# Optimization experiments

Measured on AMD Instinct MI355X. Metric: run time of the kernel, lower is better.

The kernel has to match this reference:

```python
import jax, jax.numpy as jnp
import numpy as np

N = 100000
E = 1600000
IN_C = 128
OUT_C = 64


def setup_inputs() -> dict:
    key = jax.random.key(0)
    ks = jax.random.split(key, 8)
    x = jax.random.normal(ks[0], (N, IN_C), dtype=jnp.float32)
    edge_index = jax.random.randint(ks[1], (2, E), 0, N, dtype=jnp.int64)
    neg_edge_index = jax.random.randint(ks[2], (2, E), 0, N, dtype=jnp.int64)
    # GCNConv params (glorot-ish init)
    W = jax.random.normal(ks[3], (IN_C, OUT_C), dtype=jnp.float32) / np.sqrt(IN_C)
    b = jnp.zeros((OUT_C,), dtype=jnp.float32)
    # classifier Linear(2*out_channels, 2)
    Wc = jax.random.normal(ks[4], (2 * OUT_C, 2), dtype=jnp.float32) / np.sqrt(2 * OUT_C)
    bc = jnp.zeros((2,), dtype=jnp.float32)
    return {"x": x, "edge_index": edge_index, "neg_edge_index": neg_edge_index,
            "W": W, "b": b, "Wc": Wc, "bc": bc}


def gcn_conv(x, edge_index, W, b):
    # Add self-loops, symmetric normalization: D^{-1/2} (A+I) D^{-1/2} X W + b
    loops = jnp.arange(N, dtype=edge_index.dtype)
    src = jnp.concatenate([edge_index[0], loops])  # [E+N]
    dst = jnp.concatenate([edge_index[1], loops])  # [E+N]
    deg = jax.ops.segment_sum(jnp.ones_like(dst, dtype=x.dtype), dst, num_segments=N)
    dinv = jax.lax.rsqrt(jnp.maximum(deg, 1e-12))
    norm = dinv[src] * dinv[dst]                   # [E+N]
    xw = x @ W                                     # [N, OUT_C] transform first (cheaper)
    msg = norm[:, None] * xw[src]                  # gather + scale
    out = jax.ops.segment_sum(msg, dst, num_segments=N)  # scatter-add aggregate
    return out + b


def reference(x, edge_index, neg_edge_index, W, b, Wc, bc):
    h = jax.nn.relu(gcn_conv(x, edge_index, W, b))           # [N, OUT_C]
    total = jnp.concatenate([edge_index, neg_edge_index], axis=1)  # [2, 2E]
    edge_feat = jnp.concatenate([h[total[0]], h[total[1]]], axis=1)  # [2E, 2*OUT_C]
    return edge_feat @ Wc + bc                               # [2E, 2]
```

## Files before the change

### kernel.cpp

```cpp
#include <hip/hip_runtime.h>

#define N_NODES 100000
#define N_EDGES 1600000
#define IN_C    128
#define OUT_C   64

#define SB_NODES 512
#define NSB  ((N_NODES + SB_NODES - 1) / SB_NODES)
#define SCAP 9216
#define ACHUNK 2048
#define NABLK ((N_EDGES + ACHUNK - 1) / ACHUNK)

__device__ inline unsigned pack_bf16x2(float lo, float hi) {
    unsigned a = __float_as_uint(lo), b2 = __float_as_uint(hi);
    a  += 0x7fff + ((a  >> 16) & 1);
    b2 += 0x7fff + ((b2 >> 16) & 1);
    return (a >> 16) | (b2 & 0xffff0000u);
}
__device__ inline float bf_lo(unsigned v) { return __uint_as_float(v << 16); }
__device__ inline float bf_hi(unsigned v) { return __uint_as_float(v & 0xffff0000u); }

__global__ void zero_kernel(int* __restrict__ cursor) {
    int i = blockIdx.x * blockDim.x + threadIdx.x;
    if (i < NSB) cursor[i] = 0;
}

__global__ __launch_bounds__(256) void sorta_kernel(const int* __restrict__ ei,
                                                    int* __restrict__ cursor,
                                                    int* __restrict__ sb) {
    __shared__ int histW[4][NSB];
    __shared__ int base_[NSB];
    __shared__ int cur[NSB];
    const int t = threadIdx.x, w = t >> 6;
    const long long e0 = (long long)blockIdx.x * ACHUNK;
    for (int i = t; i < 4 * NSB; i += 256) (&histW[0][0])[i] = 0;
    __syncthreads();
    const int* dsts = ei + N_EDGES;
#pragma unroll
    for (int k = 0; k < ACHUNK / 1024; ++k) {
        long long i4 = e0 / 4 + t + k * 256;
        if (i4 * 4 + 3 < N_EDGES) {
            int4 d = *(const int4*)&dsts[i4 * 4];
            atomicAdd(&histW[w][d.x >> 9], 1);
            atomicAdd(&histW[w][d.y >> 9], 1);
            atomicAdd(&histW[w][d.z >> 9], 1);
            atomicAdd(&histW[w][d.w >> 9], 1);
        }
    }
    __syncthreads();
    if (t < NSB) {
        int c = histW[0][t] + histW[1][t] + histW[2][t] + histW[3][t];
        base_[t] = c ? atomicAdd(&cursor[t], c) : 0;
        cur[t] = 0;
    }
    __syncthreads();
#pragma unroll
    for (int k = 0; k < ACHUNK / 1024; ++k) {
        long long i4 = e0 / 4 + t + k * 256;
        if (i4 * 4 + 3 < N_EDGES) {
            int4 s4 = *(const int4*)&ei[i4 * 4];
            int4 d4 = *(const int4*)&dsts[i4 * 4];
            int sv[4] = {s4.x, s4.y, s4.z, s4.w};
            int dv[4] = {d4.x, d4.y, d4.z, d4.w};
#pragma unroll
            for (int j = 0; j < 4; ++j) {
                int bk = dv[j] >> 9;
                int pos = base_[bk] + atomicAdd(&cur[bk], 1);
                if (pos < SCAP)
                    sb[bk * SCAP + pos] = sv[j] * SB_NODES + (dv[j] & (SB_NODES - 1));
            }
        }
    }
}

__global__ __launch_bounds__(1024) void sortb_kernel(const int* __restrict__ cursor,
                                                     int* __restrict__ sb,
                                                     float* __restrict__ dinv,
                                                     int* __restrict__ rowbeg,
                                                     int* __restrict__ rowend) {
    __shared__ int hist[SB_NODES];
    __shared__ int pref[SB_NODES + 1];
    __shared__ int cur[SB_NODES];
    __shared__ int sc[SB_NODES];
    __shared__ int sorted[SCAP];
    const int t = threadIdx.x, b = blockIdx.x;
    if (t < SB_NODES) { hist[t] = 0; cur[t] = 0; }
    __syncthreads();
    int m = cursor[b]; if (m > SCAP) m = SCAP;
    int* bb = sb + b * SCAP;
    for (int i = t; i < m; i += 1024) atomicAdd(&hist[bb[i] & (SB_NODES - 1)], 1);
    __syncthreads();
    if (t < SB_NODES) sc[t] = hist[t];
    __syncthreads();
    for (int off = 1; off < SB_NODES; off <<= 1) {
        int u = 0;
        if (t < SB_NODES && t >= off) u = sc[t - off];
        __syncthreads();
        if (t < SB_NODES) sc[t] += u;
        __syncthreads();
    }
    if (t < SB_NODES) pref[t] = sc[t] - hist[t];
    if (t == SB_NODES - 1) pref[SB_NODES] = sc[SB_NODES - 1];
    __syncthreads();
    for (int i = t; i < m; i += 1024) {
        int e = bb[i];
        int dl = e & (SB_NODES - 1);
        int pos = pref[dl] + atomicAdd(&cur[dl], 1);
        sorted[pos] = e >> 9;
    }
    __syncthreads();
    for (int i = t; i < m; i += 1024) bb[i] = sorted[i];
    if (t < SB_NODES) {
        int n = b * SB_NODES + t;
        if (n < N_NODES) {
            rowbeg[n] = b * SCAP + pref[t];
            rowend[n] = b * SCAP + pref[t + 1];
            dinv[n]   = rsqrtf((float)hist[t] + 1.0f);
        }
    }
}

#define XN  32
#define SXS 132
__global__ __launch_bounds__(256) void xws_kernel(const float* __restrict__ x,
                                                  const float* __restrict__ W,
                                                  const float* __restrict__ dinv,
                                                  unsigned* __restrict__ xwsh) {
    __shared__ float sW[IN_C * OUT_C];
    __shared__ float sx[XN * SXS];
    const int t = threadIdx.x;
    const int n0 = blockIdx.x * XN;
    const float4* W4 = (const float4*)W;
    float4* sW4 = (float4*)sW;
#pragma unroll
    for (int k = 0; k < 8; ++k) sW4[t + k * 256] = W4[t + k * 256];
#pragma unroll
    for (int k = 0; k < 4; ++k) {
        int idx = (t + k * 256) * 4;
        int r = idx >> 7, kk = idx & 127;
        int n = n0 + r;
        float4 v = (n < N_NODES) ? *(const float4*)&x[(long long)n * IN_C + kk]
                                 : make_float4(0.f, 0.f, 0.f, 0.f);
        *(float4*)&sx[r * SXS + kk] = v;
    }
    __syncthreads();
    const int r  = t >> 4;
    const int cq = (t & 15) << 2;
    float4 a0 = make_float4(0.f,0.f,0.f,0.f), a1 = a0;
#pragma unroll 8
    for (int k = 0; k < IN_C; ++k) {
        float x0 = sx[r * SXS + k];
        float x1 = sx[(r + 16) * SXS + k];
        float4 wv = *(const float4*)&sW[(k << 6) + cq];
        a0.x = fmaf(x0, wv.x, a0.x); a0.y = fmaf(x0, wv.y, a0.y);
        a0.z = fmaf(x0, wv.z, a0.z); a0.w = fmaf(x0, wv.w, a0.w);
        a1.x = fmaf(x1, wv.x, a1.x); a1.y = fmaf(x1, wv.y, a1.y);
        a1.z = fmaf(x1, wv.z, a1.z); a1.w = fmaf(x1, wv.w, a1.w);
    }
    int na = n0 + r, nb = n0 + r + 16;
    if (na < N_NODES) {
        float di = dinv[na];
        uint2 o = make_uint2(pack_bf16x2(a0.x * di, a0.y * di),
                             pack_bf16x2(a0.z * di, a0.w * di));
        *(uint2*)&xwsh[(long long)na * 32 + ((t & 15) << 1)] = o;
    }
    if (nb < N_NODES) {
        float di = dinv[nb];
        uint2 o = make_uint2(pack_bf16x2(a1.x * di, a1.y * di),
                             pack_bf16x2(a1.z * di, a1.w * di));
        *(uint2*)&xwsh[(long long)nb * 32 + ((t & 15) << 1)] = o;
    }
}

__global__ __launch_bounds__(256) void aggnode_kernel(
    const int* __restrict__ rowbeg, const int* __restrict__ rowend,
    const int* __restrict__ srcs, const float* __restrict__ dinv,
    const unsigned* __restrict__ xwsh, const float* __restrict__ b,
    const float* __restrict__ Wc, const float* __restrict__ bc,
    float2* __restrict__ p, float2* __restrict__ q) {
    const int lane = threadIdx.x & 63;
    const int hl   = lane & 31;
    const int g    = hl >> 3;
    const int j    = hl & 7;
    const unsigned woff = (unsigned)(j << 2);
    const int node = blockIdx.x * 8 + ((threadIdx.x >> 6) << 1) + (lane >> 5);
    const int beg = rowbeg[node], end = rowend[node];
    const float di = dinv[node];
    const uint4 vsl = *(const uint4*)&xwsh[((unsigned)node << 5) + woff];
    float a0=0.f,a1=0.f,a2=0.f,a3=0.f,a4=0.f,a5=0.f,a6=0.f,a7=0.f;
    const int m1 = end - 1;
    for (int i = beg; i < end; i += 16) {
        int e0 = i + g, e1 = e0 + 4, e2 = e0 + 8, e3 = e0 + 12;
        int i0 = min(e0, m1), i1 = min(e1, m1), i2 = min(e2, m1), i3 = min(e3, m1);
        int s0 = srcs[i0], s1 = srcs[i1], s2 = srcs[i2], s3 = srcs[i3];
        float f0 = (e0 < end) ? 1.f : 0.f;
        float f1 = (e1 < end) ? 1.f : 0.f;
        float f2 = (e2 < end) ? 1.f : 0.f;
        float f3 = (e3 < end) ? 1.f : 0.f;
        uint4 v0 = *(const uint4*)&xwsh[((unsigned)s0 << 5) + woff];
        uint4 v1 = *(const uint4*)&xwsh[((unsigned)s1 << 5) + woff];
        uint4 v2 = *(const uint4*)&xwsh[((unsigned)s2 << 5) + woff];
        uint4 v3 = *(const uint4*)&xwsh[((unsigned)s3 << 5) + woff];
        a0 = fmaf(f0, bf_lo(v0.x), a0); a1 = fmaf(f0, bf_hi(v0.x), a1);
        a2 = fmaf(f0, bf_lo(v0.y), a2); a3 = fmaf(f0, bf_hi(v0.y), a3);
        a4 = fmaf(f0, bf_lo(v0.z), a4); a5 = fmaf(f0, bf_hi(v0.z), a5);
        a6 = fmaf(f0, bf_lo(v0.w), a6); a7 = fmaf(f0, bf_hi(v0.w), a7);
        a0 = fmaf(f1, bf_lo(v1.x), a0); a1 = fmaf(f1, bf_hi(v1.x), a1);
        a2 = fmaf(f1, bf_lo(v1.y), a2); a3 = fmaf(f1, bf_hi(v1.y), a3);
        a4 = fmaf(f1, bf_lo(v1.z), a4); a5 = fmaf(f1, bf_hi(v1.z), a5);
        a6 = fmaf(f1, bf_lo(v1.w), a6); a7 = fmaf(f1, bf_hi(v1.w), a7);
        a0 = fmaf(f2, bf_lo(v2.x), a0); a1 = fmaf(f2, bf_hi(v2.x), a1);
        a2 = fmaf(f2, bf_lo(v2.y), a2); a3 = fmaf(f2, bf_hi(v2.y), a3);
        a4 = fmaf(f2, bf_lo(v2.z), a4); a5 = fmaf(f2, bf_hi(v2.z), a5);
        a6 = fmaf(f2, bf_lo(v2.w), a6); a7 = fmaf(f2, bf_hi(v2.w), a7);
        a0 = fmaf(f3, bf_lo(v3.x), a0); a1 = fmaf(f3, bf_hi(v3.x), a1);
        a2 = fmaf(f3, bf_lo(v3.y), a2); a3 = fmaf(f3, bf_hi(v3.y), a3);
        a4 = fmaf(f3, bf_lo(v3.z), a4); a5 = fmaf(f3, bf_hi(v3.z), a5);
        a6 = fmaf(f3, bf_lo(v3.w), a6); a7 = fmaf(f3, bf_hi(v3.w), a7);
    }
    a0 += __shfl_xor(a0, 8); a0 += __shfl_xor(a0, 16);
    a1 += __shfl_xor(a1, 8); a1 += __shfl_xor(a1, 16);
    a2 += __shfl_xor(a2, 8); a2 += __shfl_xor(a2, 16);
    a3 += __shfl_xor(a3, 8); a3 += __shfl_xor(a3, 16);
    a4 += __shfl_xor(a4, 8); a4 += __shfl_xor(a4, 16);
    a5 += __shfl_xor(a5, 8); a5 += __shfl_xor(a5, 16);
    a6 += __shfl_xor(a6, 8); a6 += __shfl_xor(a6, 16);
    a7 += __shfl_xor(a7, 8); a7 += __shfl_xor(a7, 16);
    a0 += bf_lo(vsl.x); a1 += bf_hi(vsl.x);
    a2 += bf_lo(vsl.y); a3 += bf_hi(vsl.y);
    a4 += bf_lo(vsl.z); a5 += bf_hi(vsl.z);
    a6 += bf_lo(vsl.w); a7 += bf_hi(vsl.w);
    float4 bA = ((const float4*)b)[(j << 1)];
    float4 bB = ((const float4*)b)[(j << 1) + 1];
    float h0 = fmaxf(fmaf(di, a0, bA.x), 0.f);
    float h1 = fmaxf(fmaf(di, a1, bA.y), 0.f);
    float h2 = fmaxf(fmaf(di, a2, bA.z), 0.f);
    float h3 = fmaxf(fmaf(di, a3, bA.w), 0.f);
    float h4 = fmaxf(fmaf(di, a4, bB.x), 0.f);
    float h5 = fmaxf(fmaf(di, a5, bB.y), 0.f);
    float h6 = fmaxf(fmaf(di, a6, bB.z), 0.f);
    float h7 = fmaxf(fmaf(di, a7, bB.w), 0.f);
    const float4* WS = (const float4*)Wc;
    const float4* WD = (const float4*)(Wc + 2 * OUT_C);
    float p0, p1, q0, q1;
    {
        float4 w0 = WS[(j << 2)], w1 = WS[(j << 2) + 1];
        float4 w2 = WS[(j << 2) + 2], w3 = WS[(j << 2) + 3];
        p0 = h0 * w0.x + h1 * w0.z + h2 * w1.x + h3 * w1.z
           + h4 * w2.x + h5 * w2.z + h6 * w3.x + h7 * w3.z;
        p1 = h0 * w0.y + h1 * w0.w + h2 * w1.y + h3 * w1.w
           + h4 * w2.y + h5 * w2.w + h6 * w3.y + h7 * w3.w;
    }
    {
        float4 u0 = WD[(j << 2)], u1 = WD[(j << 2) + 1];
        float4 u2 = WD[(j << 2) + 2], u3 = WD[(j << 2) + 3];
        q0 = h0 * u0.x + h1 * u0.z + h2 * u1.x + h3 * u1.z
           + h4 * u2.x + h5 * u2.z + h6 * u3.x + h7 * u3.z;
        q1 = h0 * u0.y + h1 * u0.w + h2 * u1.y + h3 * u1.w
           + h4 * u2.y + h5 * u2.w + h6 * u3.y + h7 * u3.w;
    }
#pragma unroll
    for (int off = 1; off <= 4; off <<= 1) {
        p0 += __shfl_xor(p0, off); p1 += __shfl_xor(p1, off);
        q0 += __shfl_xor(q0, off); q1 += __shfl_xor(q1, off);
    }
    if (hl == 0) {
        p[node] = make_float2(p0 + bc[0], p1 + bc[1]);
        q[node] = make_float2(q0, q1);
    }
}

__global__ __launch_bounds__(256) void edge_kernel(
    const int* __restrict__ ei, const int* __restrict__ nei,
    const float2* __restrict__ p, const float2* __restrict__ q,
    float4* __restrict__ out4) {
    int idx = blockIdx.x * blockDim.x + threadIdx.x;
    if (idx >= 2 * N_EDGES / 8) return;
    int e8 = idx * 8;
    const int *S, *D;
    int off;
    if (e8 < N_EDGES) { S = ei;  D = ei  + N_EDGES; off = e8; }
    else              { S = nei; D = nei + N_EDGES; off = e8 - N_EDGES; }
    int4 sA = *(const int4*)&S[off];
    int4 sB = *(const int4*)&S[off + 4];
    int4 dA = *(const int4*)&D[off];
    int4 dB = *(const int4*)&D[off + 4];
    float2 p0 = p[sA.x], p1 = p[sA.y], p2 = p[sA.z], p3 = p[sA.w];
    float2 p4 = p[sB.x], p5 = p[sB.y], p6 = p[sB.z], p7 = p[sB.w];
    float2 q0 = q[dA.x], q1 = q[dA.y], q2 = q[dA.z], q3 = q[dA.w];
    float2 q4 = q[dB.x], q5 = q[dB.y], q6 = q[dB.z], q7 = q[dB.w];
    out4[idx * 4 + 0] = make_float4(p0.x + q0.x, p0.y + q0.y, p1.x + q1.x, p1.y + q1.y);
    out4[idx * 4 + 1] = make_float4(p2.x + q2.x, p2.y + q2.y, p3.x + q3.x, p3.y + q3.y);
    out4[idx * 4 + 2] = make_float4(p4.x + q4.x, p4.y + q4.y, p5.x + q5.x, p5.y + q5.y);
    out4[idx * 4 + 3] = make_float4(p6.x + q6.x, p6.y + q6.y, p7.x + q7.x, p7.y + q7.y);
}

extern "C" void kernel_launch(void* const* d_in, const int* in_sizes, int n_in,
                              void* d_out, int out_size, void* d_ws, size_t ws_size,
                              hipStream_t stream) {
    const float* x   = (const float*)d_in[0];
    const int*   ei  = (const int*)  d_in[1];
    const int*   nei = (const int*)  d_in[2];
    const float* W   = (const float*)d_in[3];
    const float* b   = (const float*)d_in[4];
    const float* Wc  = (const float*)d_in[5];
    const float* bc  = (const float*)d_in[6];

    int*      wsI    = (int*)d_ws;
    float*    dinv   = (float*)wsI;
    unsigned* xwsh   = (unsigned*)(wsI + 100352);
    float*    p      = (float*)(wsI + 3300352);
    float*    q      = (float*)(wsI + 3501056);
    int*      cursor = wsI + 3701760;
    int*      rowbeg = wsI + 3702016;
    int*      rowend = wsI + 3802368;
    int*      sbuf   = wsI + 3902720;

    const int B = 256;
    zero_kernel<<<1, B, 0, stream>>>(cursor);
    sorta_kernel<<<NABLK, B, 0, stream>>>(ei, cursor, sbuf);
    sortb_kernel<<<NSB, 1024, 0, stream>>>(cursor, sbuf, dinv, rowbeg, rowend);
    xws_kernel<<<(N_NODES + XN - 1) / XN, B, 0, stream>>>(x, W, dinv, xwsh);
    aggnode_kernel<<<N_NODES / 8, B, 0, stream>>>(rowbeg, rowend, sbuf, dinv, xwsh,
                                                  b, Wc, bc, (float2*)p, (float2*)q);
    edge_kernel<<<(2 * N_EDGES / 8 + B - 1) / B, B, 0, stream>>>(
        ei, nei, (const float2*)p, (const float2*)q, (float4*)d_out);
}
```

Before: 254.8 us.

## Replace two-level bucket sort with global-atomic degree histogram and scatter CSR build

Swaps the two-pass shared-memory bucket sort (superblock bucketing followed by an in-block sort) for a simpler CSR build. A global atomic degree histogram feeds a per-chunk prefix scan with fixed chunk capacity, and a scatter kernel then places each edge source using global atomics on per-node cursors. This removes the local sorting and shared-memory staging but puts heavy global atomic traffic on 100k counters. The edge order within each row also becomes nondeterministic, and a chunk that overflows CHCAP is not guarded.

```diff
diff --git a/kernel.cpp b/kernel.cpp
--- a/kernel.cpp
+++ b/kernel.cpp
@@ -5,11 +5,8 @@
 #define IN_C    128
 #define OUT_C   64
 
-#define SB_NODES 512
-#define NSB  ((N_NODES + SB_NODES - 1) / SB_NODES)
-#define SCAP 9216
-#define ACHUNK 2048
-#define NABLK ((N_EDGES + ACHUNK - 1) / ACHUNK)
+#define NCHUNK 98
+#define CHCAP  17408
 
 __device__ inline unsigned pack_bf16x2(float lo, float hi) {
     unsigned a = __float_as_uint(lo), b2 = __float_as_uint(hi);
@@ -20,104 +17,57 @@
 __device__ inline float bf_lo(unsigned v) { return __uint_as_float(v << 16); }
 __device__ inline float bf_hi(unsigned v) { return __uint_as_float(v & 0xffff0000u); }
 
-__global__ void zero_kernel(int* __restrict__ cursor) {
+__global__ void zero_kernel(int* __restrict__ deg) {
     int i = blockIdx.x * blockDim.x + threadIdx.x;
-    if (i < NSB) cursor[i] = 0;
-}
-
-__global__ __launch_bounds__(256) void sorta_kernel(const int* __restrict__ ei,
-                                                    int* __restrict__ cursor,
-                                                    int* __restrict__ sb) {
-    __shared__ int histW[4][NSB];
-    __shared__ int base_[NSB];
-    __shared__ int cur[NSB];
-    const int t = threadIdx.x, w = t >> 6;
-    const long long e0 = (long long)blockIdx.x * ACHUNK;
-    for (int i = t; i < 4 * NSB; i += 256) (&histW[0][0])[i] = 0;
+    if (i < N_NODES) deg[i] = 0;
+}
+
+__global__ __launch_bounds__(256) void hist_kernel(const int* __restrict__ dsts,
+                                                   int* __restrict__ deg) {
+    int idx = blockIdx.x * blockDim.x + threadIdx.x;
+    if (idx >= N_EDGES / 4) return;
+    int4 d4 = *(const int4*)&dsts[idx * 4];
+    atomicAdd(&deg[d4.x], 1);
+    atomicAdd(&deg[d4.y], 1);
+    atomicAdd(&deg[d4.z], 1);
+    atomicAdd(&deg[d4.w], 1);
+}
+
+__global__ __launch_bounds__(1024) void chunkscan_kernel(const int* __restrict__ deg,
+                                                         int* __restrict__ rowbeg,
+                                                         int* __restrict__ rend,
+                                                         float* __restrict__ dinv) {
+    __shared__ int sc[1024];
+    const int t = threadIdx.x;
+    const int n = blockIdx.x * 1024 + t;
+    int d = (n < N_NODES) ? deg[n] : 0;
+    sc[t] = d;
     __syncthreads();
-    const int* dsts = ei + N_EDGES;
-#pragma unroll
-    for (int k = 0; k < ACHUNK / 1024; ++k) {
-        long long i4 = e0 / 4 + t + k * 256;
-        if (i4 * 4 + 3 < N_EDGES) {
-            int4 d = *(const int4*)&dsts[i4 * 4];
-            atomicAdd(&histW[w][d.x >> 9], 1);
-            atomicAdd(&histW[w][d.y >> 9], 1);
-            atomicAdd(&histW[w][d.z >> 9], 1);
-            atomicAdd(&histW[w][d.w >> 9], 1);
-        }
-    }
-    __syncthreads();
-    if (t < NSB) {
-        int c = histW[0][t] + histW[1][t] + histW[2][t] + histW[3][t];
-        base_[t] = c ? atomicAdd(&cursor[t], c) : 0;
-        cur[t] = 0;
-    }
-    __syncthreads();
-#pragma unroll
-    for (int k = 0; k < ACHUNK / 1024; ++k) {
-        long long i4 = e0 / 4 + t + k * 256;
-        if (i4 * 4 + 3 < N_EDGES) {
-            int4 s4 = *(const int4*)&ei[i4 * 4];
-            int4 d4 = *(const int4*)&dsts[i4 * 4];
-            int sv[4] = {s4.x, s4.y, s4.z, s4.w};
-            int dv[4] = {d4.x, d4.y, d4.z, d4.w};
-#pragma unroll
-            for (int j = 0; j < 4; ++j) {
-                int bk = dv[j] >> 9;
-                int pos = base_[bk] + atomicAdd(&cur[bk], 1);
-                if (pos < SCAP)
-                    sb[bk * SCAP + pos] = sv[j] * SB_NODES + (dv[j] & (SB_NODES - 1));
-            }
-        }
-    }
-}
-
-__global__ __launch_bounds__(1024) void sortb_kernel(const int* __restrict__ cursor,
-                                                     int* __restrict__ sb,
-                                                     float* __restrict__ dinv,
-                                                     int* __restrict__ rowbeg,
-                                                     int* __restrict__ rowend) {
-    __shared__ int hist[SB_NODES];
-    __shared__ int pref[SB_NODES + 1];
-    __shared__ int cur[SB_NODES];
-    __shared__ int sc[SB_NODES];
-    __shared__ int sorted[SCAP];
-    const int t = threadIdx.x, b = blockIdx.x;
-    if (t < SB_NODES) { hist[t] = 0; cur[t] = 0; }
-    __syncthreads();
-    int m = cursor[b]; if (m > SCAP) m = SCAP;
-    int* bb = sb + b * SCAP;
-    for (int i = t; i < m; i += 1024) atomicAdd(&hist[bb[i] & (SB_NODES - 1)], 1);
-    __syncthreads();
-    if (t < SB_NODES) sc[t] = hist[t];
-    __syncthreads();
-    for (int off = 1; off < SB_NODES; off <<= 1) {
-        int u = 0;
-        if (t < SB_NODES && t >= off) u = sc[t - off];
+    for (int off = 1; off < 1024; off <<= 1) {
+        int u = (t >= off) ? sc[t - off] : 0;
         __syncthreads();
-        if (t < SB_NODES) sc[t] += u;
+        sc[t] += u;
         __syncthreads();
     }
-    if (t < SB_NODES) pref[t] = sc[t] - hist[t];
-    if (t == SB_NODES - 1) pref[SB_NODES] = sc[SB_NODES - 1];
-    __syncthreads();
-    for (int i = t; i < m; i += 1024) {
-        int e = bb[i];
-        int dl = e & (SB_NODES - 1);
-        int pos = pref[dl] + atomicAdd(&cur[dl], 1);
-        sorted[pos] = e >> 9;
-    }
-    __syncthreads();
-    for (int i = t; i < m; i += 1024) bb[i] = sorted[i];
-    if (t < SB_NODES) {
-        int n = b * SB_NODES + t;
-        if (n < N_NODES) {
-            rowbeg[n] = b * SCAP + pref[t];
-            rowend[n] = b * SCAP + pref[t + 1];
-            dinv[n]   = rsqrtf((float)hist[t] + 1.0f);
-        }
-    }
+    if (n < N_NODES) {
+        int base = blockIdx.x * CHCAP + sc[t] - d;
+        rowbeg[n] = base;
+        rend[n]   = base;
+        dinv[n]   = rsqrtf((float)d + 1.0f);
+    }
+}
+
+__global__ __launch_bounds__(256) void scatter_kernel(const int* __restrict__ ei,
+                                                      int* __restrict__ rend,
+                                                      int* __restrict__ csr) {
+    int idx = blockIdx.x * blockDim.x + threadIdx.x;
+    if (idx >= N_EDGES / 4) return;
+    int4 s4 = *(const int4*)&ei[idx * 4];
+    int4 d4 = *(const int4*)&ei[N_EDGES + idx * 4];
+    int p0 = atomicAdd(&rend[d4.x], 1); csr[p0] = s4.x;
+    int p1 = atomicAdd(&rend[d4.y], 1); csr[p1] = s4.y;
+    int p2 = atomicAdd(&rend[d4.z], 1); csr[p2] = s4.z;
+    int p3 = atomicAdd(&rend[d4.w], 1); csr[p3] = s4.w;
 }
 
 #define XN  32
@@ -311,17 +261,18 @@
     unsigned* xwsh   = (unsigned*)(wsI + 100352);
     float*    p      = (float*)(wsI + 3300352);
     float*    q      = (float*)(wsI + 3501056);
-    int*      cursor = wsI + 3701760;
-    int*      rowbeg = wsI + 3702016;
-    int*      rowend = wsI + 3802368;
-    int*      sbuf   = wsI + 3902720;
+    int*      deg    = wsI + 3701760;
+    int*      rowbeg = wsI + 3802112;
+    int*      rend   = wsI + 3902464;
+    int*      csr    = wsI + 4002816;
 
     const int B = 256;
-    zero_kernel<<<1, B, 0, stream>>>(cursor);
-    sorta_kernel<<<NABLK, B, 0, stream>>>(ei, cursor, sbuf);
-    sortb_kernel<<<NSB, 1024, 0, stream>>>(cursor, sbuf, dinv, rowbeg, rowend);
+    zero_kernel<<<(N_NODES + B - 1) / B, B, 0, stream>>>(deg);
+    hist_kernel<<<(N_EDGES / 4 + B - 1) / B, B, 0, stream>>>(ei + N_EDGES, deg);
+    chunkscan_kernel<<<NCHUNK, 1024, 0, stream>>>(deg, rowbeg, rend, dinv);
+    scatter_kernel<<<(N_EDGES / 4 + B - 1) / B, B, 0, stream>>>(ei, rend, csr);
     xws_kernel<<<(N_NODES + XN - 1) / XN, B, 0, stream>>>(x, W, dinv, xwsh);
-    aggnode_kernel<<<N_NODES / 8, B, 0, stream>>>(rowbeg, rowend, sbuf, dinv, xwsh,
+    aggnode_kernel<<<N_NODES / 8, B, 0, stream>>>(rowbeg, rend, csr, dinv, xwsh,
                                                   b, Wc, bc, (float2*)p, (float2*)q);
     edge_kernel<<<(2 * N_EDGES / 8 + B - 1) / B, B, 0, stream>>>(
         ei, nei, (const float2*)p, (const float2*)q, (float4*)d_out);
```

Result: slower. 413.5 us (+62.2%).
